# Performance work log

Hardware: AMD Instinct MI355X
Metric: run time of the kernel (lower is better)

Reference implementation:

```python
import jax, jax.numpy as jnp
import numpy as np

B, T, D, N = 256, 512, 512, 64


def setup_inputs() -> dict:
    key = jax.random.key(0)
    ks = jax.random.split(key, 8)
    s = 0.05  # keep gate pre-activations in a sane range
    return {
        "x": jax.random.normal(ks[0], (B, T, D), dtype=jnp.float32),
        "init_h": jax.random.normal(ks[1], (B, D), dtype=jnp.float32) * s,
        "W_ih": jax.random.normal(ks[2], (4 * D, D + N), dtype=jnp.float32) * s,
        "b_ih": jax.random.normal(ks[3], (4 * D,), dtype=jnp.float32) * s,
        "W_hh": jax.random.normal(ks[4], (4 * D, D), dtype=jnp.float32) * s,
        "b_hh": jax.random.normal(ks[5], (4 * D,), dtype=jnp.float32) * s,
        "W_lin": jax.random.normal(ks[6], (N, D), dtype=jnp.float32) * s,
        "b_lin": jax.random.normal(ks[7], (N,), dtype=jnp.float32) * s,
    }


def reference(x, init_h, W_ih, b_ih, W_hh, b_hh, W_lin, b_lin):
    n_class = W_lin.shape[0]
    d = init_h.shape[-1]

    def step(carry, x_t):
        h, c, y = carry
        inp = jnp.concatenate([x_t, y], axis=-1)  # [B, D+N]
        gates = inp @ W_ih.T + b_ih + h @ W_hh.T + b_hh  # [B, 4D]
        i, f, g, o = jnp.split(gates, 4, axis=-1)
        i = jax.nn.sigmoid(i)
        f = jax.nn.sigmoid(f)
        g = jnp.tanh(g)
        o = jax.nn.sigmoid(o)
        c = f * c + i * g
        h = o * jnp.tanh(c)
        y = jax.nn.softmax(h @ W_lin.T + b_lin, axis=-1)  # [B, N]
        return (h, c, y), y

    c0 = jnp.zeros_like(init_h)
    y0 = jnp.zeros((x.shape[0], n_class), dtype=x.dtype)
    xs = jnp.swapaxes(x, 0, 1)  # [T, B, D]
    _, ys = jax.lax.scan(step, (init_h, c0, y0), xs)  # ys: [T, B, N]
    return jnp.swapaxes(ys, 0, 1)  # [B, T, N]
```

## Files before the change

kernel.cpp:

```cpp
#include <hip/hip_runtime.h>
#include <cstdint>
#include <cstddef>


typedef _Float16 f16x8 __attribute__((ext_vector_type(8)));
typedef float f32x4 __attribute__((ext_vector_type(4)));
typedef unsigned long long u64;

#define MFMA16(a, b, c_) __builtin_amdgcn_mfma_f32_16x16x32_f16((a), (b), (c_), 0, 0, 0)
#define AGT __HIP_MEMORY_SCOPE_AGENT
#define RLX __ATOMIC_RELAXED

#define FLAG_INTS (256 * 64 + 64)
#define HS2_U32 131072

static __device__ __forceinline__ unsigned short f2b(_Float16 h) {
  return __builtin_bit_cast(unsigned short, h);
}
static __device__ __forceinline__ _Float16 b2f(unsigned short s) {
  return __builtin_bit_cast(_Float16, s);
}

__device__ __forceinline__ void cvt8(const float4 a, const float4 b, f16x8& hi, f16x8& lo) {
  float v[8] = {a.x, a.y, a.z, a.w, b.x, b.y, b.z, b.w};
#pragma unroll
  for (int j = 0; j < 8; ++j) {
    _Float16 h = (_Float16)v[j];
    hi[j] = h;
    lo[j] = (_Float16)(v[j] - (float)h);
  }
}

template <bool XPRE>
__global__ void prep_kernel(const float* __restrict__ x, const float* __restrict__ init_h,
                            const float* __restrict__ W_ih, const float* __restrict__ b_ih,
                            const float* __restrict__ W_hh, const float* __restrict__ b_hh,
                            const float* __restrict__ W_lin, _Float16* __restrict__ xs,
                            _Float16* __restrict__ wf_hi, _Float16* __restrict__ wf_lo,
                            _Float16* __restrict__ wlf_hi, unsigned int* __restrict__ hs2,
                            float* __restrict__ bias, int* __restrict__ flags) {
  const long NX = XPRE ? 256L * 512 * 16 * 4 : 0;
  const int NWF = 128 * 34 * 64;
  const int NWLF = 4 * 16 * 64;
  const int NH2 = 256 * 128;
  long tid = (long)blockIdx.x * 256 + threadIdx.x;

  if (XPRE && tid < NX) {
    int q = tid & 3, ki = (tid >> 2) & 15, t = (tid >> 6) & 511;
    int row = (int)(tid >> 15);
    const float* s = x + (((size_t)row * 512 + t) * 512 + ki * 32 + 4 * q);
    float4 a = *(const float4*)s, b = *(const float4*)(s + 16);
    f16x8 hi, lo;
    cvt8(a, b, hi, lo);
    _Float16* d = xs + ((((size_t)row * 512 + t) * 16 + ki) * 64 + q * 16);
    *(f16x8*)d = hi;
    *(f16x8*)(d + 8) = lo;
    return;
  }
  long u = tid - NX;
  if (u >= 0 && u < NWF) {
    int l = (int)(u & 63);
    int u2 = (int)(u >> 6);
    int ki = u2 % 34, ct = u2 / 34;
    int cb = ct >> 1, cth = ct & 1;
    int l15 = l & 15;
    int col = (l15 >> 2) * 512 + cb * 8 + cth * 4 + (l15 & 3);
    int k = ki * 32 + 4 * (l >> 4);
    float4 a, b;
    if (k < 512) {
      const float* p = W_ih + (size_t)col * 576;
      a = *(const float4*)(p + k);
      b = *(const float4*)(p + k + 16);
    } else if (k < 1024) {
      const float* p = W_hh + (size_t)col * 512;
      a = *(const float4*)(p + k - 512);
      b = *(const float4*)(p + k - 512 + 16);
    } else {
      const float* p = W_ih + (size_t)col * 576 + 512;
      a = *(const float4*)(p + k - 1024);
      b = *(const float4*)(p + k - 1024 + 16);
    }
    f16x8 hi, lo;
    cvt8(a, b, hi, lo);
    size_t idx = (((size_t)ct * 34 + ki) * 64 + l) * 8;
    *(f16x8*)(wf_hi + idx) = hi;
    *(f16x8*)(wf_lo + idx) = lo;
    return;
  }
  u -= NWF;
  if (u >= 0 && u < NWLF) {
    int l = (int)(u & 63);
    int u2 = (int)(u >> 6);
    int ki = u2 & 15, ct = u2 >> 4;
    int col = ct * 16 + (l & 15);
    int k = ki * 32 + 4 * (l >> 4);
    const float* p = W_lin + (size_t)col * 512;
    float4 a = *(const float4*)(p + k), b = *(const float4*)(p + k + 16);
    f16x8 hi, lo;
    cvt8(a, b, hi, lo);
    _Float16* dh = wlf_hi + ((size_t)(ct * 16 + ki) * 64 + l) * 8;
    *(f16x8*)dh = hi;
    return;
  }
  u -= NWLF;
  if (u >= 0 && u < NH2) {
    int g4 = (int)(u & 127), row = (int)(u >> 7);
    const float* s = init_h + (size_t)row * 512 + g4 * 4;
    float4 a = *(const float4*)s;
    float v[4] = {a.x, a.y, a.z, a.w};
    unsigned int* d = hs2 + (size_t)row * 512 + g4 * 4;
#pragma unroll
    for (int j = 0; j < 4; ++j) {
      _Float16 hh = (_Float16)v[j];
      _Float16 hl = (_Float16)(v[j] - (float)hh);
      d[j] = (unsigned int)f2b(hh) | ((unsigned int)f2b(hl) << 16);
    }
    return;
  }
  u -= NH2;
  if (u >= 0 && u < 2048) {
    bias[u] = b_ih[u] + b_hh[u];
    return;
  }
  u -= 2048;
  if (u >= 0 && u < FLAG_INTS) flags[u] = 0;
}

template <bool XPRE>
__global__ void __launch_bounds__(512, 1) recur_kernel(
    const float* __restrict__ x, const float* __restrict__ b_lin,
    const _Float16* __restrict__ xs, const _Float16* __restrict__ wf_hi,
    const _Float16* __restrict__ wf_lo, const _Float16* __restrict__ wlf_hi,
    unsigned int* __restrict__ hs2, const float* __restrict__ bias, float* __restrict__ out,
    int* __restrict__ flags) {
  const int bid = blockIdx.x;
  const int x8 = bid & 7;
  const int g = x8 >> 1;
  const int cb = (x8 & 1) * 32 + (bid >> 3);
  const int tid = threadIdx.x;
  const int l = tid & 63, w = tid >> 6;
  const int l15 = l & 15, q = l >> 4;
  const int kh = w & 1, rtp = w >> 1;

  __shared__ _Float16 wfl_hi[2 * 34 * 64 * 8];
  __shared__ _Float16 wlin_h[4 * 16 * 64 * 8];
  __shared__ float scratch[4608];
  __shared__ int s_ab;

  {
    const _Float16* srcw = wf_hi + (size_t)(2 * cb) * 17408;
#pragma unroll
    for (int i = 0; i < 9; ++i) {
      int u = tid + i * 512;
      if (u < 4352) *(float4*)(wfl_hi + (size_t)u * 8) = *(const float4*)(srcw + (size_t)u * 8);
    }
#pragma unroll
    for (int i = 0; i < 8; ++i) {
      int u = tid + i * 512;
      *(float4*)(wlin_h + (size_t)u * 8) = *(const float4*)(wlf_hi + (size_t)u * 8);
    }
    if (tid == 0) s_ab = 0;
  }
  __syncthreads();

  const int dd = l15 & 3, rr = l15 >> 2;
  float bg[2][4];
#pragma unroll
  for (int c2 = 0; c2 < 2; ++c2)
#pragma unroll
    for (int gi = 0; gi < 4; ++gi) bg[c2][gi] = bias[gi * 512 + cb * 8 + c2 * 4 + dd];
  const float blv0 = b_lin[l15], blv1 = b_lin[16 + l15];
  const float blv2 = b_lin[32 + l15], blv3 = b_lin[48 + l15];

  const int Rw = g * 64 + rtp * 16;
  const int rowA = Rw + l15;
  const _Float16* xsA = xs + (size_t)rowA * 524288 + q * 16;
  const float* xfA = x + (size_t)rowA * 262144 + 4 * q;
  const unsigned int* hldA = hs2 + (size_t)rowA * 512 + 4 * q;
  const int rowE = Rw + 4 * q + rr;

  const _Float16* wflo_b = wf_lo + (size_t)(2 * cb) * 17408 + (size_t)l * 8;

  int* abortf = flags + 256 * 64;

  auto ARRIVE = [&](int v) {
    __syncthreads();
    if (tid == 0) __hip_atomic_store(flags + (size_t)(g * 64 + cb) * 64, v, RLX, AGT);
  };
  auto WAIT = [&](int v) -> bool {
    if (tid < 64) {
      int a = 0;
      int* f = flags + ((size_t)g * 64 + tid) * 64;
      int it = 0;
      while (__hip_atomic_load(f, RLX, AGT) < v) {
        __builtin_amdgcn_s_sleep(1);
        if (++it > 400000) {
          a = 1;
          break;
        }
        if ((it & 255) == 0 && __hip_atomic_load(abortf, RLX, AGT) != 0) {
          a = 1;
          break;
        }
      }
      a = __any(a) ? 1 : 0;
      if (tid == 0) {
        if (a) __hip_atomic_store(abortf, 1, RLX, AGT);
        s_ab = a;
      }
    }
    __syncthreads();
    return s_ab != 0;
  };

  auto GK3 = [&](const f16x8& ah, const f16x8& al, int KI, f32x4& A0, f32x4& A1) {
    const _Float16* ph0 = wfl_hi + ((size_t)KI * 64 + l) * 8;
    const _Float16* ph1 = ph0 + 17408;
    const _Float16* pl0 = wflo_b + (size_t)KI * 512;
    const _Float16* pl1 = pl0 + 17408;
    f16x8 b0h = *(const f16x8*)ph0, b1h = *(const f16x8*)ph1;
    f16x8 b0l = *(const f16x8*)pl0, b1l = *(const f16x8*)pl1;
    A0 = MFMA16(ah, b0h, A0);
    A1 = MFMA16(ah, b1h, A1);
    A0 = MFMA16(al, b0h, A0);
    A1 = MFMA16(al, b1h, A1);
    A0 = MFMA16(ah, b0l, A0);
    A1 = MFMA16(ah, b1l, A1);
  };
  auto XGEMM = [&](int t, f32x4& A0, f32x4& A1) {
    if (XPRE) {
      const _Float16* xA = xsA + (size_t)t * 1024;
#pragma unroll
      for (int i = 0; i < 8; ++i) {
        int kx = kh * 8 + i;
        f16x8 ah = *(const f16x8*)(xA + kx * 64);
        f16x8 al = *(const f16x8*)(xA + kx * 64 + 8);
        GK3(ah, al, kx, A0, A1);
      }
    } else {
      const float* xp = xfA + (size_t)t * 512;
#pragma unroll 2
      for (int i = 0; i < 8; ++i) {
        int kx = kh * 8 + i;
        float4 av = *(const float4*)(xp + kx * 32);
        float4 bv = *(const float4*)(xp + kx * 32 + 16);
        f16x8 ah, al;
        cvt8(av, bv, ah, al);
        GK3(ah, al, kx, A0, A1);
      }
    }
  };

  const f32x4 Z = {0.f, 0.f, 0.f, 0.f};
  float cst[2] = {0.f, 0.f};
  f32x4 aC0 = Z, aC1 = Z;
  XGEMM(0, aC0, aC1);

  const int ctW = cb >> 4, lW = cb & 15;

#pragma unroll 1
  for (int s = 0; s < 512; ++s) {
    if (s > 0) {
      if (WAIT(s)) return;
    }

    f16x8 hh[8], hl[8];
    const unsigned int* hp0 = hldA + (size_t)(s & 1) * HS2_U32;
#pragma unroll
    for (int i = 0; i < 8; ++i) {
      const unsigned int* hp = hp0 + (kh * 8 + i) * 32;
      u64 u0 = __hip_atomic_load((const u64*)hp, RLX, AGT);
      u64 u1 = __hip_atomic_load((const u64*)(hp + 2), RLX, AGT);
      u64 u2 = __hip_atomic_load((const u64*)(hp + 16), RLX, AGT);
      u64 u3 = __hip_atomic_load((const u64*)(hp + 18), RLX, AGT);
      unsigned int wd[8] = {(unsigned int)u0, (unsigned int)(u0 >> 32),
                            (unsigned int)u1, (unsigned int)(u1 >> 32),
                            (unsigned int)u2, (unsigned int)(u2 >> 32),
                            (unsigned int)u3, (unsigned int)(u3 >> 32)};
#pragma unroll
      for (int j = 0; j < 8; ++j) {
        hh[i][j] = b2f((unsigned short)(wd[j] & 0xffffu));
        hl[i][j] = b2f((unsigned short)(wd[j] >> 16));
      }
    }

    f32x4 y0 = Z, y1 = Z, y2 = Z, y3 = Z;
    if (s > 0) {
#pragma unroll
      for (int i = 0; i < 8; ++i) {
        int ki = kh * 8 + i;
        const _Float16* ph0 = wlin_h + ((size_t)(0 * 16 + ki) * 64 + l) * 8;
        const _Float16* ph1 = wlin_h + ((size_t)(1 * 16 + ki) * 64 + l) * 8;
        const _Float16* ph2 = wlin_h + ((size_t)(2 * 16 + ki) * 64 + l) * 8;
        const _Float16* ph3 = wlin_h + ((size_t)(3 * 16 + ki) * 64 + l) * 8;
        f16x8 b0 = *(const f16x8*)ph0, b1 = *(const f16x8*)ph1;
        f16x8 b2 = *(const f16x8*)ph2, b3 = *(const f16x8*)ph3;
        y0 = MFMA16(hh[i], b0, y0);
        y1 = MFMA16(hh[i], b1, y1);
        y2 = MFMA16(hh[i], b2, y2);
        y3 = MFMA16(hh[i], b3, y3);
        y0 = MFMA16(hl[i], b0, y0);
        y1 = MFMA16(hl[i], b1, y1);
        y2 = MFMA16(hl[i], b2, y2);
        y3 = MFMA16(hl[i], b3, y3);
      }
    }
#pragma unroll
    for (int i = 0; i < 8; ++i) GK3(hh[i], hl[i], 16 + kh * 8 + i, aC0, aC1);

    if (s > 0) {
      if (kh == 1) {
#pragma unroll
        for (int r = 0; r < 4; ++r) {
          scratch[((rtp * 4 + 0) * 4 + r) * 64 + l] = y0[r];
          scratch[((rtp * 4 + 1) * 4 + r) * 64 + l] = y1[r];
          scratch[((rtp * 4 + 2) * 4 + r) * 64 + l] = y2[r];
          scratch[((rtp * 4 + 3) * 4 + r) * 64 + l] = y3[r];
        }
      }
      __syncthreads();
      float la0[4], la1[4], la2[4], la3[4];
      if (kh == 0) {
#pragma unroll
        for (int r = 0; r < 4; ++r) {
          la0[r] = y0[r] + scratch[((rtp * 4 + 0) * 4 + r) * 64 + l] + blv0;
          la1[r] = y1[r] + scratch[((rtp * 4 + 1) * 4 + r) * 64 + l] + blv1;
          la2[r] = y2[r] + scratch[((rtp * 4 + 2) * 4 + r) * 64 + l] + blv2;
          la3[r] = y3[r] + scratch[((rtp * 4 + 3) * 4 + r) * 64 + l] + blv3;
        }
#pragma unroll
        for (int r = 0; r < 4; ++r) {
          float mx = fmaxf(fmaxf(la0[r], la1[r]), fmaxf(la2[r], la3[r]));
          mx = fmaxf(mx, __shfl_xor(mx, 1));
          mx = fmaxf(mx, __shfl_xor(mx, 2));
          mx = fmaxf(mx, __shfl_xor(mx, 4));
          mx = fmaxf(mx, __shfl_xor(mx, 8));
          float e0 = __expf(la0[r] - mx), e1 = __expf(la1[r] - mx);
          float e2 = __expf(la2[r] - mx), e3 = __expf(la3[r] - mx);
          float sm = e0 + e1 + e2 + e3;
          sm += __shfl_xor(sm, 1);
          sm += __shfl_xor(sm, 2);
          sm += __shfl_xor(sm, 4);
          sm += __shfl_xor(sm, 8);
          float inv = 1.f / sm;
          la0[r] = e0 * inv;
          la1[r] = e1 * inv;
          la2[r] = e2 * inv;
          la3[r] = e3 * inv;
        }
        if (l15 == lW) {
#pragma unroll
          for (int r = 0; r < 4; ++r) {
            float vv = (ctW == 0) ? la0[r] : (ctW == 1) ? la1[r] : (ctW == 2) ? la2[r] : la3[r];
            out[((size_t)(g * 64 + rtp * 16 + 4 * q + r) * 512 + (s - 1)) * 64 + cb] = vv;
          }
        }
      }
      __syncthreads();
      if (kh == 0) {
        _Float16* yt = (_Float16*)scratch;
#pragma unroll
        for (int r = 0; r < 4; ++r) {
          int row = rtp * 16 + 4 * q + r;
          float v[4] = {la0[r], la1[r], la2[r], la3[r]};
#pragma unroll
          for (int ct = 0; ct < 4; ++ct) {
            _Float16 vh = (_Float16)v[ct];
            _Float16 vl = (_Float16)(v[ct] - (float)vh);
            yt[row * 136 + ct * 16 + l15] = vh;
            yt[row * 136 + 72 + ct * 16 + l15] = vl;
          }
        }
      }
      __syncthreads();
      {
        const _Float16* yt = (const _Float16*)scratch + (rtp * 16 + l15) * 136 + kh * 32 + 4 * q;
        union {
          u64 d[2];
          f16x8 v;
        } th, tl;
        th.d[0] = *(const u64*)yt;
        th.d[1] = *(const u64*)(yt + 16);
        tl.d[0] = *(const u64*)(yt + 72);
        tl.d[1] = *(const u64*)(yt + 88);
        GK3(th.v, tl.v, 32 + kh, aC0, aC1);
      }
      __syncthreads();
    }

    if (kh == 1) {
#pragma unroll
      for (int r = 0; r < 4; ++r) {
        scratch[((rtp * 2 + 0) * 4 + r) * 64 + l] = aC0[r];
        scratch[((rtp * 2 + 1) * 4 + r) * 64 + l] = aC1[r];
      }
    }
    __syncthreads();
    if (kh == 0) {
#pragma unroll
      for (int r = 0; r < 4; ++r) {
        aC0[r] += scratch[((rtp * 2 + 0) * 4 + r) * 64 + l];
        aC1[r] += scratch[((rtp * 2 + 1) * 4 + r) * 64 + l];
      }
#pragma unroll
      for (int c2 = 0; c2 < 2; ++c2) {
        f32x4 A = c2 ? aC1 : aC0;
        float z[4];
#pragma unroll
        for (int gi = 0; gi < 4; ++gi) {
          int src = (l & 48) | (gi * 4 + dd);
          float v0 = __shfl(A[0], src), v1 = __shfl(A[1], src);
          float v2 = __shfl(A[2], src), v3 = __shfl(A[3], src);
          z[gi] = (rr == 0) ? v0 : (rr == 1) ? v1 : (rr == 2) ? v2 : v3;
        }
        float zi = z[0] + bg[c2][0], zf = z[1] + bg[c2][1];
        float zg = z[2] + bg[c2][2], zo = z[3] + bg[c2][3];
        float iv = 1.f / (1.f + __expf(-zi));
        float fv = 1.f / (1.f + __expf(-zf));
        float eg = __expf(2.f * zg);
        float gv = 1.f - 2.f / (eg + 1.f);
        float ov = 1.f / (1.f + __expf(-zo));
        float cn = fv * cst[c2] + iv * gv;
        cst[c2] = cn;
        float ec = __expf(2.f * cn);
        float th2 = 1.f - 2.f / (ec + 1.f);
        float hv = ov * th2;
        _Float16 hhv = (_Float16)hv;
        _Float16 hlv = (_Float16)(hv - (float)hhv);
        unsigned int pk = (unsigned int)f2b(hhv) | ((unsigned int)f2b(hlv) << 16);
        int dglob = cb * 8 + c2 * 4 + dd;
        __hip_atomic_store(hs2 + (size_t)((s + 1) & 1) * HS2_U32 + rowE * 512 + dglob, pk, RLX,
                           AGT);
      }
    }
    ARRIVE(s + 1);
    if (s < 511) {
      f32x4 aN0 = Z, aN1 = Z;
      XGEMM(s + 1, aN0, aN1);
      aC0 = aN0;
      aC1 = aN1;
    }
  }

  if (WAIT(512)) return;
  {
    f16x8 hh[8], hl[8];
    const unsigned int* hp0 = hldA;
#pragma unroll
    for (int i = 0; i < 8; ++i) {
      const unsigned int* hp = hp0 + (kh * 8 + i) * 32;
      u64 u0 = __hip_atomic_load((const u64*)hp, RLX, AGT);
      u64 u1 = __hip_atomic_load((const u64*)(hp + 2), RLX, AGT);
      u64 u2 = __hip_atomic_load((const u64*)(hp + 16), RLX, AGT);
      u64 u3 = __hip_atomic_load((const u64*)(hp + 18), RLX, AGT);
      unsigned int wd[8] = {(unsigned int)u0, (unsigned int)(u0 >> 32),
                            (unsigned int)u1, (unsigned int)(u1 >> 32),
                            (unsigned int)u2, (unsigned int)(u2 >> 32),
                            (unsigned int)u3, (unsigned int)(u3 >> 32)};
#pragma unroll
      for (int j = 0; j < 8; ++j) {
        hh[i][j] = b2f((unsigned short)(wd[j] & 0xffffu));
        hl[i][j] = b2f((unsigned short)(wd[j] >> 16));
      }
    }
    f32x4 y0 = Z, y1 = Z, y2 = Z, y3 = Z;
#pragma unroll
    for (int i = 0; i < 8; ++i) {
      int ki = kh * 8 + i;
      const _Float16* ph0 = wlin_h + ((size_t)(0 * 16 + ki) * 64 + l) * 8;
      const _Float16* ph1 = wlin_h + ((size_t)(1 * 16 + ki) * 64 + l) * 8;
      const _Float16* ph2 = wlin_h + ((size_t)(2 * 16 + ki) * 64 + l) * 8;
      const _Float16* ph3 = wlin_h + ((size_t)(3 * 16 + ki) * 64 + l) * 8;
      f16x8 b0 = *(const f16x8*)ph0, b1 = *(const f16x8*)ph1;
      f16x8 b2 = *(const f16x8*)ph2, b3 = *(const f16x8*)ph3;
      y0 = MFMA16(hh[i], b0, y0);
      y1 = MFMA16(hh[i], b1, y1);
      y2 = MFMA16(hh[i], b2, y2);
      y3 = MFMA16(hh[i], b3, y3);
      y0 = MFMA16(hl[i], b0, y0);
      y1 = MFMA16(hl[i], b1, y1);
      y2 = MFMA16(hl[i], b2, y2);
      y3 = MFMA16(hl[i], b3, y3);
    }
    if (kh == 1) {
#pragma unroll
      for (int r = 0; r < 4; ++r) {
        scratch[((rtp * 4 + 0) * 4 + r) * 64 + l] = y0[r];
        scratch[((rtp * 4 + 1) * 4 + r) * 64 + l] = y1[r];
        scratch[((rtp * 4 + 2) * 4 + r) * 64 + l] = y2[r];
        scratch[((rtp * 4 + 3) * 4 + r) * 64 + l] = y3[r];
      }
    }
    __syncthreads();
    if (kh == 0) {
      float la0[4], la1[4], la2[4], la3[4];
#pragma unroll
      for (int r = 0; r < 4; ++r) {
        la0[r] = y0[r] + scratch[((rtp * 4 + 0) * 4 + r) * 64 + l] + blv0;
        la1[r] = y1[r] + scratch[((rtp * 4 + 1) * 4 + r) * 64 + l] + blv1;
        la2[r] = y2[r] + scratch[((rtp * 4 + 2) * 4 + r) * 64 + l] + blv2;
        la3[r] = y3[r] + scratch[((rtp * 4 + 3) * 4 + r) * 64 + l] + blv3;
      }
#pragma unroll
      for (int r = 0; r < 4; ++r) {
        float mx = fmaxf(fmaxf(la0[r], la1[r]), fmaxf(la2[r], la3[r]));
        mx = fmaxf(mx, __shfl_xor(mx, 1));
        mx = fmaxf(mx, __shfl_xor(mx, 2));
        mx = fmaxf(mx, __shfl_xor(mx, 4));
        mx = fmaxf(mx, __shfl_xor(mx, 8));
        float e0 = __expf(la0[r] - mx), e1 = __expf(la1[r] - mx);
        float e2 = __expf(la2[r] - mx), e3 = __expf(la3[r] - mx);
        float sm = e0 + e1 + e2 + e3;
        sm += __shfl_xor(sm, 1);
        sm += __shfl_xor(sm, 2);
        sm += __shfl_xor(sm, 4);
        sm += __shfl_xor(sm, 8);
        float inv = 1.f / sm;
        la0[r] = e0 * inv;
        la1[r] = e1 * inv;
        la2[r] = e2 * inv;
        la3[r] = e3 * inv;
      }
      if (l15 == lW) {
#pragma unroll
        for (int r = 0; r < 4; ++r) {
          float vv = (ctW == 0) ? la0[r] : (ctW == 1) ? la1[r] : (ctW == 2) ? la2[r] : la3[r];
          out[((size_t)(g * 64 + rtp * 16 + 4 * q + r) * 512 + 511) * 64 + cb] = vv;
        }
      }
    }
  }
}

extern "C" void kernel_launch(void* const* d_in, const int* in_sizes, int n_in, void* d_out,
                              int out_size, void* d_ws, size_t ws_size, hipStream_t stream) {
  const float* x = (const float*)d_in[0];
  const float* init_h = (const float*)d_in[1];
  const float* W_ih = (const float*)d_in[2];
  const float* b_ih = (const float*)d_in[3];
  const float* W_hh = (const float*)d_in[4];
  const float* b_hh = (const float*)d_in[5];
  const float* W_lin = (const float*)d_in[6];
  const float* b_lin = (const float*)d_in[7];
  float* out = (float*)d_out;
  (void)in_sizes;
  (void)n_in;
  (void)out_size;

  char* ws = (char*)d_ws;
  size_t off = 0;
  auto take = [&](size_t bytes) -> char* {
    char* r = ws + off;
    off = (off + bytes + 255) & ~(size_t)255;
    return r;
  };
  const size_t WFP_E = (size_t)128 * 34 * 64 * 8;
  const size_t WLF_E = (size_t)4 * 16 * 64 * 8;
  const size_t XS_E = (size_t)256 * 512 * 16 * 64;

  _Float16* wf_hi = (_Float16*)take(WFP_E * 2);
  _Float16* wf_lo = (_Float16*)take(WFP_E * 2);
  _Float16* wlf_hi = (_Float16*)take(WLF_E * 2);
  unsigned int* hs2 = (unsigned int*)take((size_t)2 * HS2_U32 * 4);
  float* bias = (float*)take(2048 * 4);
  int* flags = (int*)take((size_t)FLAG_INTS * 4);
  if (ws_size < off) return;
  _Float16* xs = (_Float16*)(ws + off);
  const bool xpre = (ws_size >= off + XS_E * 2);

  if (xpre) {
    const long total = 8388608L + 278528 + 4096 + 32768 + 2048 + FLAG_INTS;
    prep_kernel<true><<<(int)((total + 255) / 256), 256, 0, stream>>>(
        x, init_h, W_ih, b_ih, W_hh, b_hh, W_lin, xs, wf_hi, wf_lo, wlf_hi, hs2, bias, flags);
    recur_kernel<true><<<256, 512, 0, stream>>>(x, b_lin, xs, wf_hi, wf_lo, wlf_hi, hs2, bias,
                                                out, flags);
  } else {
    const long total = 278528L + 4096 + 32768 + 2048 + FLAG_INTS;
    prep_kernel<false><<<(int)((total + 255) / 256), 256, 0, stream>>>(
        x, init_h, W_ih, b_ih, W_hh, b_hh, W_lin, xs, wf_hi, wf_lo, wlf_hi, hs2, bias, flags);
    recur_kernel<false><<<256, 512, 0, stream>>>(x, b_lin, xs, wf_hi, wf_lo, wlf_hi, hs2, bias,
                                                 out, flags);
  }
}
```

Baseline: 9.623 ms.

## Partition LSTM recurrence per XCD with local sync groups and hi/lo LDS weights

Each block reads its XCD id from a hardware register and takes a slot through an atomic counter. Groups of 32 blocks on the same XCD then share batch rows, so the per-step flag barrier and hidden-state exchange stay within one XCD's L2. Recurrent weights (W_hh plus the feedback part of W_ih) are stored interleaved as hi/lo in LDS. The input-projection weights are now read from global memory. The softmax feedback GEMM is done by half the waves, with W_lin read from global. Atomics become volatile accesses and x gets nontemporal loads. The kernel aborts if the XCD mapping does not yield exactly 32 blocks per XCD. It depends on the hardware block placement and on volatile ordering being correct for cross-block visibility.

```diff
diff --git a/kernel.cpp b/kernel.cpp
--- a/kernel.cpp
+++ b/kernel.cpp
@@ -5,14 +5,17 @@
 
 typedef _Float16 f16x8 __attribute__((ext_vector_type(8)));
 typedef float f32x4 __attribute__((ext_vector_type(4)));
+typedef unsigned int u32x4 __attribute__((ext_vector_type(4)));
 typedef unsigned long long u64;
 
 #define MFMA16(a, b, c_) __builtin_amdgcn_mfma_f32_16x16x32_f16((a), (b), (c_), 0, 0, 0)
 #define AGT __HIP_MEMORY_SCOPE_AGENT
 #define RLX __ATOMIC_RELAXED
 
-#define FLAG_INTS (256 * 64 + 64)
 #define HS2_U32 131072
+#define ABORT_OFF 16384
+#define XCDCNT_OFF 16448
+#define FLAG_INTS 16456
 
 static __device__ __forceinline__ unsigned short f2b(_Float16 h) {
   return __builtin_bit_cast(unsigned short, h);
@@ -36,9 +39,10 @@
                             const float* __restrict__ W_ih, const float* __restrict__ b_ih,
                             const float* __restrict__ W_hh, const float* __restrict__ b_hh,
                             const float* __restrict__ W_lin, _Float16* __restrict__ xs,
-                            _Float16* __restrict__ wf_hi, _Float16* __restrict__ wf_lo,
-                            _Float16* __restrict__ wlf_hi, unsigned int* __restrict__ hs2,
-                            float* __restrict__ bias, int* __restrict__ flags) {
+                            _Float16* __restrict__ wx_hi, _Float16* __restrict__ wx_lo,
+                            _Float16* __restrict__ whl, _Float16* __restrict__ wlf_hi,
+                            unsigned int* __restrict__ hs2, float* __restrict__ bias,
+                            int* __restrict__ flags) {
   const long NX = XPRE ? 256L * 512 * 16 * 4 : 0;
   const int NWF = 128 * 34 * 64;
   const int NWLF = 4 * 16 * 64;
@@ -61,10 +65,9 @@
   if (u >= 0 && u < NWF) {
     int l = (int)(u & 63);
     int u2 = (int)(u >> 6);
-    int ki = u2 % 34, ct = u2 / 34;
-    int cb = ct >> 1, cth = ct & 1;
-    int l15 = l & 15;
-    int col = (l15 >> 2) * 512 + cb * 8 + cth * 4 + (l15 & 3);
+    int ki = u2 % 34, sl = u2 / 34;
+    int gate = sl & 3, c = sl >> 2;
+    int col = gate * 512 + c * 16 + (l & 15);
     int k = ki * 32 + 4 * (l >> 4);
     float4 a, b;
     if (k < 512) {
@@ -82,9 +85,15 @@
     }
     f16x8 hi, lo;
     cvt8(a, b, hi, lo);
-    size_t idx = (((size_t)ct * 34 + ki) * 64 + l) * 8;
-    *(f16x8*)(wf_hi + idx) = hi;
-    *(f16x8*)(wf_lo + idx) = lo;
+    if (ki < 16) {
+      size_t idx = (((size_t)sl * 16 + ki) * 64 + l) * 8;
+      *(f16x8*)(wx_hi + idx) = hi;
+      *(f16x8*)(wx_lo + idx) = lo;
+    } else {
+      size_t idx = (((size_t)sl * 18 + (ki - 16)) * 64 + l) * 16;
+      *(f16x8*)(whl + idx) = hi;
+      *(f16x8*)(whl + idx + 8) = lo;
+    }
     return;
   }
   u -= NWF;
@@ -98,8 +107,7 @@
     float4 a = *(const float4*)(p + k), b = *(const float4*)(p + k + 16);
     f16x8 hi, lo;
     cvt8(a, b, hi, lo);
-    _Float16* dh = wlf_hi + ((size_t)(ct * 16 + ki) * 64 + l) * 8;
-    *(f16x8*)dh = hi;
+    *(f16x8*)(wlf_hi + ((size_t)(ct * 16 + ki) * 64 + l) * 8) = hi;
     return;
   }
   u -= NWLF;
@@ -129,72 +137,70 @@
 template <bool XPRE>
 __global__ void __launch_bounds__(512, 1) recur_kernel(
     const float* __restrict__ x, const float* __restrict__ b_lin,
-    const _Float16* __restrict__ xs, const _Float16* __restrict__ wf_hi,
-    const _Float16* __restrict__ wf_lo, const _Float16* __restrict__ wlf_hi,
-    unsigned int* __restrict__ hs2, const float* __restrict__ bias, float* __restrict__ out,
-    int* __restrict__ flags) {
-  const int bid = blockIdx.x;
-  const int x8 = bid & 7;
-  const int g = x8 >> 1;
-  const int cb = (x8 & 1) * 32 + (bid >> 3);
+    const _Float16* __restrict__ xs, const _Float16* __restrict__ wx_hi,
+    const _Float16* __restrict__ wx_lo, const _Float16* __restrict__ whl,
+    const _Float16* __restrict__ wlf_hi, unsigned int* __restrict__ hs2,
+    const float* __restrict__ bias, float* __restrict__ out, int* __restrict__ flags) {
   const int tid = threadIdx.x;
   const int l = tid & 63, w = tid >> 6;
   const int l15 = l & 15, q = l >> 4;
-  const int kh = w & 1, rtp = w >> 1;
-
-  __shared__ _Float16 wfl_hi[2 * 34 * 64 * 8];
-  __shared__ _Float16 wlin_h[4 * 16 * 64 * 8];
-  __shared__ float scratch[4608];
-  __shared__ int s_ab;
+  const int kh = w & 1, rt = (w >> 1) & 1, ch = w >> 2;
+
+  __shared__ _Float16 whl_lds[73728];
+  __shared__ float scratch[2304];
+  __shared__ int s_ab, s_g, s_c;
+
+  if (tid == 0) {
+    s_ab = 0;
+    int xcc = __builtin_amdgcn_s_getreg(63508) & 7;
+    int slot = __hip_atomic_fetch_add(flags + XCDCNT_OFF + xcc, 1, RLX, AGT);
+    s_g = xcc;
+    s_c = slot;
+    if (slot >= 32) {
+      __hip_atomic_store(flags + ABORT_OFF, 1, RLX, AGT);
+      s_ab = 1;
+    }
+  }
+  __syncthreads();
+  if (s_ab) return;
+  const int g = s_g, c = s_c;
+  const int ct0 = ch * 2, ct1 = ch * 2 + 1;
 
   {
-    const _Float16* srcw = wf_hi + (size_t)(2 * cb) * 17408;
-#pragma unroll
-    for (int i = 0; i < 9; ++i) {
-      int u = tid + i * 512;
-      if (u < 4352) *(float4*)(wfl_hi + (size_t)u * 8) = *(const float4*)(srcw + (size_t)u * 8);
-    }
-#pragma unroll
-    for (int i = 0; i < 8; ++i) {
-      int u = tid + i * 512;
-      *(float4*)(wlin_h + (size_t)u * 8) = *(const float4*)(wlf_hi + (size_t)u * 8);
-    }
-    if (tid == 0) s_ab = 0;
+    const _Float16* src = whl + (size_t)c * 73728;
+#pragma unroll
+    for (int i = 0; i < 18; ++i) {
+      int uu = tid + i * 512;
+      *(float4*)(whl_lds + (size_t)uu * 8) = *(const float4*)(src + (size_t)uu * 8);
+    }
   }
   __syncthreads();
 
-  const int dd = l15 & 3, rr = l15 >> 2;
-  float bg[2][4];
-#pragma unroll
-  for (int c2 = 0; c2 < 2; ++c2)
-#pragma unroll
-    for (int gi = 0; gi < 4; ++gi) bg[c2][gi] = bias[gi * 512 + cb * 8 + c2 * 4 + dd];
+  float bg[4];
+#pragma unroll
+  for (int gi = 0; gi < 4; ++gi) bg[gi] = bias[gi * 512 + c * 16 + l15];
   const float blv0 = b_lin[l15], blv1 = b_lin[16 + l15];
   const float blv2 = b_lin[32 + l15], blv3 = b_lin[48 + l15];
 
-  const int Rw = g * 64 + rtp * 16;
-  const int rowA = Rw + l15;
+  const int rowA = g * 32 + rt * 16 + l15;
   const _Float16* xsA = xs + (size_t)rowA * 524288 + q * 16;
   const float* xfA = x + (size_t)rowA * 262144 + 4 * q;
   const unsigned int* hldA = hs2 + (size_t)rowA * 512 + 4 * q;
-  const int rowE = Rw + 4 * q + rr;
-
-  const _Float16* wflo_b = wf_lo + (size_t)(2 * cb) * 17408 + (size_t)l * 8;
-
-  int* abortf = flags + 256 * 64;
+
+  int* abortf = flags + ABORT_OFF;
 
   auto ARRIVE = [&](int v) {
     __syncthreads();
-    if (tid == 0) __hip_atomic_store(flags + (size_t)(g * 64 + cb) * 64, v, RLX, AGT);
+    if (tid == 0) *(volatile int*)(flags + (size_t)(g * 32 + c) * 64) = v;
   };
   auto WAIT = [&](int v) -> bool {
-    if (tid < 64) {
+    if (tid < 32) {
       int a = 0;
-      int* f = flags + ((size_t)g * 64 + tid) * 64;
+      volatile int* f = (volatile int*)(flags + ((size_t)g * 32 + tid) * 64);
       int it = 0;
-      while (__hip_atomic_load(f, RLX, AGT) < v) {
+      while (*f < v) {
         __builtin_amdgcn_s_sleep(1);
-        if (++it > 400000) {
+        if (++it > 300000) {
           a = 1;
           break;
         }
@@ -213,13 +219,23 @@
     return s_ab != 0;
   };
 
-  auto GK3 = [&](const f16x8& ah, const f16x8& al, int KI, f32x4& A0, f32x4& A1) {
-    const _Float16* ph0 = wfl_hi + ((size_t)KI * 64 + l) * 8;
-    const _Float16* ph1 = ph0 + 17408;
-    const _Float16* pl0 = wflo_b + (size_t)KI * 512;
-    const _Float16* pl1 = pl0 + 17408;
-    f16x8 b0h = *(const f16x8*)ph0, b1h = *(const f16x8*)ph1;
-    f16x8 b0l = *(const f16x8*)pl0, b1l = *(const f16x8*)pl1;
+  auto GKH = [&](const f16x8& ah, const f16x8& al, int kidx, f32x4& A0, f32x4& A1) {
+    const _Float16* p0 = whl_lds + (((size_t)ct0 * 18 + kidx) * 64 + l) * 16;
+    const _Float16* p1 = whl_lds + (((size_t)ct1 * 18 + kidx) * 64 + l) * 16;
+    f16x8 b0h = *(const f16x8*)p0, b0l = *(const f16x8*)(p0 + 8);
+    f16x8 b1h = *(const f16x8*)p1, b1l = *(const f16x8*)(p1 + 8);
+    A0 = MFMA16(ah, b0h, A0);
+    A1 = MFMA16(ah, b1h, A1);
+    A0 = MFMA16(al, b0h, A0);
+    A1 = MFMA16(al, b1h, A1);
+    A0 = MFMA16(ah, b0l, A0);
+    A1 = MFMA16(ah, b1l, A1);
+  };
+  auto GKX = [&](const f16x8& ah, const f16x8& al, int ki, f32x4& A0, f32x4& A1) {
+    size_t i0 = (((size_t)(c * 4 + ct0) * 16 + ki) * 64 + l) * 8;
+    size_t i1 = (((size_t)(c * 4 + ct1) * 16 + ki) * 64 + l) * 8;
+    f16x8 b0h = *(const f16x8*)(wx_hi + i0), b0l = *(const f16x8*)(wx_lo + i0);
+    f16x8 b1h = *(const f16x8*)(wx_hi + i1), b1l = *(const f16x8*)(wx_lo + i1);
     A0 = MFMA16(ah, b0h, A0);
     A1 = MFMA16(ah, b1h, A1);
     A0 = MFMA16(al, b0h, A0);
@@ -233,9 +249,13 @@
 #pragma unroll
       for (int i = 0; i < 8; ++i) {
         int kx = kh * 8 + i;
-        f16x8 ah = *(const f16x8*)(xA + kx * 64);
-        f16x8 al = *(const f16x8*)(xA + kx * 64 + 8);
-        GK3(ah, al, kx, A0, A1);
+        union {
+          u32x4 u;
+          f16x8 v;
+        } ua, ub;
+        ua.u = __builtin_nontemporal_load((const u32x4*)(xA + kx * 64));
+        ub.u = __builtin_nontemporal_load((const u32x4*)(xA + kx * 64 + 8));
+        GKX(ua.v, ub.v, kx, A0, A1);
       }
     } else {
       const float* xp = xfA + (size_t)t * 512;
@@ -246,17 +266,15 @@
         float4 bv = *(const float4*)(xp + kx * 32 + 16);
         f16x8 ah, al;
         cvt8(av, bv, ah, al);
-        GK3(ah, al, kx, A0, A1);
+        GKX(ah, al, kx, A0, A1);
       }
     }
   };
 
   const f32x4 Z = {0.f, 0.f, 0.f, 0.f};
-  float cst[2] = {0.f, 0.f};
+  float cst[4] = {0.f, 0.f, 0.f, 0.f};
   f32x4 aC0 = Z, aC1 = Z;
   XGEMM(0, aC0, aC1);
-
-  const int ctW = cb >> 4, lW = cb & 15;
 
 #pragma unroll 1
   for (int s = 0; s < 512; ++s) {
@@ -269,10 +287,10 @@
 #pragma unroll
     for (int i = 0; i < 8; ++i) {
       const unsigned int* hp = hp0 + (kh * 8 + i) * 32;
-      u64 u0 = __hip_atomic_load((const u64*)hp, RLX, AGT);
-      u64 u1 = __hip_atomic_load((const u64*)(hp + 2), RLX, AGT);
-      u64 u2 = __hip_atomic_load((const u64*)(hp + 16), RLX, AGT);
-      u64 u3 = __hip_atomic_load((const u64*)(hp + 18), RLX, AGT);
+      u64 u0 = *(const volatile u64*)hp;
+      u64 u1 = *(const volatile u64*)(hp + 2);
+      u64 u2 = *(const volatile u64*)(hp + 16);
+      u64 u3 = *(const volatile u64*)(hp + 18);
       unsigned int wd[8] = {(unsigned int)u0, (unsigned int)(u0 >> 32),
                             (unsigned int)u1, (unsigned int)(u1 >> 32),
                             (unsigned int)u2, (unsigned int)(u2 >> 32),
@@ -285,16 +303,14 @@
     }
 
     f32x4 y0 = Z, y1 = Z, y2 = Z, y3 = Z;
-    if (s > 0) {
+    if (s > 0 && ch == 0) {
 #pragma unroll
       for (int i = 0; i < 8; ++i) {
         int ki = kh * 8 + i;
-        const _Float16* ph0 = wlin_h + ((size_t)(0 * 16 + ki) * 64 + l) * 8;
-        const _Float16* ph1 = wlin_h + ((size_t)(1 * 16 + ki) * 64 + l) * 8;
-        const _Float16* ph2 = wlin_h + ((size_t)(2 * 16 + ki) * 64 + l) * 8;
-        const _Float16* ph3 = wlin_h + ((size_t)(3 * 16 + ki) * 64 + l) * 8;
-        f16x8 b0 = *(const f16x8*)ph0, b1 = *(const f16x8*)ph1;
-        f16x8 b2 = *(const f16x8*)ph2, b3 = *(const f16x8*)ph3;
+        f16x8 b0 = *(const f16x8*)(wlf_hi + (((size_t)(0 * 16 + ki)) * 64 + l) * 8);
+        f16x8 b1 = *(const f16x8*)(wlf_hi + (((size_t)(1 * 16 + ki)) * 64 + l) * 8);
+        f16x8 b2 = *(const f16x8*)(wlf_hi + (((size_t)(2 * 16 + ki)) * 64 + l) * 8);
+        f16x8 b3 = *(const f16x8*)(wlf_hi + (((size_t)(3 * 16 + ki)) * 64 + l) * 8);
         y0 = MFMA16(hh[i], b0, y0);
         y1 = MFMA16(hh[i], b1, y1);
         y2 = MFMA16(hh[i], b2, y2);
@@ -306,67 +322,66 @@
       }
     }
 #pragma unroll
-    for (int i = 0; i < 8; ++i) GK3(hh[i], hl[i], 16 + kh * 8 + i, aC0, aC1);
+    for (int i = 0; i < 8; ++i) GKH(hh[i], hl[i], kh * 8 + i, aC0, aC1);
 
     if (s > 0) {
-      if (kh == 1) {
+      if (ch == 0 && kh == 1) {
 #pragma unroll
         for (int r = 0; r < 4; ++r) {
-          scratch[((rtp * 4 + 0) * 4 + r) * 64 + l] = y0[r];
-          scratch[((rtp * 4 + 1) * 4 + r) * 64 + l] = y1[r];
-          scratch[((rtp * 4 + 2) * 4 + r) * 64 + l] = y2[r];
-          scratch[((rtp * 4 + 3) * 4 + r) * 64 + l] = y3[r];
+          scratch[((rt * 4 + 0) * 4 + r) * 64 + l] = y0[r];
+          scratch[((rt * 4 + 1) * 4 + r) * 64 + l] = y1[r];
+          scratch[((rt * 4 + 2) * 4 + r) * 64 + l] = y2[r];
+          scratch[((rt * 4 + 3) * 4 + r) * 64 + l] = y3[r];
         }
       }
       __syncthreads();
-      float la0[4], la1[4], la2[4], la3[4];
-      if (kh == 0) {
+      if (ch == 0 && kh == 0) {
+        float la[4][4];
 #pragma unroll
         for (int r = 0; r < 4; ++r) {
-          la0[r] = y0[r] + scratch[((rtp * 4 + 0) * 4 + r) * 64 + l] + blv0;
-          la1[r] = y1[r] + scratch[((rtp * 4 + 1) * 4 + r) * 64 + l] + blv1;
-          la2[r] = y2[r] + scratch[((rtp * 4 + 2) * 4 + r) * 64 + l] + blv2;
-          la3[r] = y3[r] + scratch[((rtp * 4 + 3) * 4 + r) * 64 + l] + blv3;
+          la[0][r] = y0[r] + scratch[((rt * 4 + 0) * 4 + r) * 64 + l] + blv0;
+          la[1][r] = y1[r] + scratch[((rt * 4 + 1) * 4 + r) * 64 + l] + blv1;
+          la[2][r] = y2[r] + scratch[((rt * 4 + 2) * 4 + r) * 64 + l] + blv2;
+          la[3][r] = y3[r] + scratch[((rt * 4 + 3) * 4 + r) * 64 + l] + blv3;
         }
 #pragma unroll
         for (int r = 0; r < 4; ++r) {
-          float mx = fmaxf(fmaxf(la0[r], la1[r]), fmaxf(la2[r], la3[r]));
+          float mx = fmaxf(fmaxf(la[0][r], la[1][r]), fmaxf(la[2][r], la[3][r]));
           mx = fmaxf(mx, __shfl_xor(mx, 1));
           mx = fmaxf(mx, __shfl_xor(mx, 2));
           mx = fmaxf(mx, __shfl_xor(mx, 4));
           mx = fmaxf(mx, __shfl_xor(mx, 8));
-          float e0 = __expf(la0[r] - mx), e1 = __expf(la1[r] - mx);
-          float e2 = __expf(la2[r] - mx), e3 = __expf(la3[r] - mx);
+          float e0 = __expf(la[0][r] - mx), e1 = __expf(la[1][r] - mx);
+          float e2 = __expf(la[2][r] - mx), e3 = __expf(la[3][r] - mx);
           float sm = e0 + e1 + e2 + e3;
           sm += __shfl_xor(sm, 1);
           sm += __shfl_xor(sm, 2);
           sm += __shfl_xor(sm, 4);
           sm += __shfl_xor(sm, 8);
           float inv = 1.f / sm;
-          la0[r] = e0 * inv;
-          la1[r] = e1 * inv;
-          la2[r] = e2 * inv;
-          la3[r] = e3 * inv;
-        }
-        if (l15 == lW) {
-#pragma unroll
-          for (int r = 0; r < 4; ++r) {
-            float vv = (ctW == 0) ? la0[r] : (ctW == 1) ? la1[r] : (ctW == 2) ? la2[r] : la3[r];
-            out[((size_t)(g * 64 + rtp * 16 + 4 * q + r) * 512 + (s - 1)) * 64 + cb] = vv;
+          la[0][r] = e0 * inv;
+          la[1][r] = e1 * inv;
+          la[2][r] = e2 * inv;
+          la[3][r] = e3 * inv;
+        }
+#pragma unroll
+        for (int j2 = 0; j2 < 2; ++j2) {
+          int n = 2 * c + j2;
+          if (l15 == (n & 15)) {
+#pragma unroll
+            for (int r = 0; r < 4; ++r)
+              out[((size_t)(g * 32 + rt * 16 + 4 * q + r) * 512 + (s - 1)) * 64 + n] =
+                  la[n >> 4][r];
           }
         }
-      }
-      __syncthreads();
-      if (kh == 0) {
         _Float16* yt = (_Float16*)scratch;
 #pragma unroll
         for (int r = 0; r < 4; ++r) {
-          int row = rtp * 16 + 4 * q + r;
-          float v[4] = {la0[r], la1[r], la2[r], la3[r]};
+          int row = rt * 16 + 4 * q + r;
 #pragma unroll
           for (int ct = 0; ct < 4; ++ct) {
-            _Float16 vh = (_Float16)v[ct];
-            _Float16 vl = (_Float16)(v[ct] - (float)vh);
+            _Float16 vh = (_Float16)la[ct][r];
+            _Float16 vl = (_Float16)(la[ct][r] - (float)vh);
             yt[row * 136 + ct * 16 + l15] = vh;
             yt[row * 136 + 72 + ct * 16 + l15] = vl;
           }
@@ -374,7 +389,7 @@
       }
       __syncthreads();
       {
-        const _Float16* yt = (const _Float16*)scratch + (rtp * 16 + l15) * 136 + kh * 32 + 4 * q;
+        const _Float16* yt = (const _Float16*)scratch + (rt * 16 + l15) * 136 + kh * 32 + 4 * q;
         union {
           u64 d[2];
           f16x8 v;
@@ -383,7 +398,7 @@
         th.d[1] = *(const u64*)(yt + 16);
         tl.d[0] = *(const u64*)(yt + 72);
         tl.d[1] = *(const u64*)(yt + 88);
-        GK3(th.v, tl.v, 32 + kh, aC0, aC1);
+        GKH(th.v, tl.v, 16 + kh, aC0, aC1);
       }
       __syncthreads();
     }
@@ -391,46 +406,50 @@
     if (kh == 1) {
 #pragma unroll
       for (int r = 0; r < 4; ++r) {
-        scratch[((rtp * 2 + 0) * 4 + r) * 64 + l] = aC0[r];
-        scratch[((rtp * 2 + 1) * 4 + r) * 64 + l] = aC1[r];
+        scratch[((rt * 4 + ct0) * 4 + r) * 64 + l] = aC0[r];
+        scratch[((rt * 4 + ct1) * 4 + r) * 64 + l] = aC1[r];
       }
     }
     __syncthreads();
     if (kh == 0) {
 #pragma unroll
       for (int r = 0; r < 4; ++r) {
-        aC0[r] += scratch[((rtp * 2 + 0) * 4 + r) * 64 + l];
-        aC1[r] += scratch[((rtp * 2 + 1) * 4 + r) * 64 + l];
-      }
-#pragma unroll
-      for (int c2 = 0; c2 < 2; ++c2) {
-        f32x4 A = c2 ? aC1 : aC0;
-        float z[4];
-#pragma unroll
-        for (int gi = 0; gi < 4; ++gi) {
-          int src = (l & 48) | (gi * 4 + dd);
-          float v0 = __shfl(A[0], src), v1 = __shfl(A[1], src);
-          float v2 = __shfl(A[2], src), v3 = __shfl(A[3], src);
-          z[gi] = (rr == 0) ? v0 : (rr == 1) ? v1 : (rr == 2) ? v2 : v3;
-        }
-        float zi = z[0] + bg[c2][0], zf = z[1] + bg[c2][1];
-        float zg = z[2] + bg[c2][2], zo = z[3] + bg[c2][3];
+        aC0[r] += scratch[((rt * 4 + ct0) * 4 + r) * 64 + l];
+        aC1[r] += scratch[((rt * 4 + ct1) * 4 + r) * 64 + l];
+      }
+      if (ch == 1) {
+#pragma unroll
+        for (int r = 0; r < 4; ++r) {
+          scratch[((rt * 4 + 2) * 4 + r) * 64 + l] = aC0[r];
+          scratch[((rt * 4 + 3) * 4 + r) * 64 + l] = aC1[r];
+        }
+      }
+    }
+    __syncthreads();
+    if (kh == 0 && ch == 0) {
+      const unsigned int wbuf = (unsigned int)(((s + 1) & 1) * HS2_U32);
+      const int dglob = c * 16 + l15;
+#pragma unroll
+      for (int r = 0; r < 4; ++r) {
+        float zi = aC0[r] + bg[0];
+        float zf = aC1[r] + bg[1];
+        float zg = scratch[((rt * 4 + 2) * 4 + r) * 64 + l] + bg[2];
+        float zo = scratch[((rt * 4 + 3) * 4 + r) * 64 + l] + bg[3];
         float iv = 1.f / (1.f + __expf(-zi));
         float fv = 1.f / (1.f + __expf(-zf));
         float eg = __expf(2.f * zg);
         float gv = 1.f - 2.f / (eg + 1.f);
         float ov = 1.f / (1.f + __expf(-zo));
-        float cn = fv * cst[c2] + iv * gv;
-        cst[c2] = cn;
+        float cn = fv * cst[r] + iv * gv;
+        cst[r] = cn;
         float ec = __expf(2.f * cn);
         float th2 = 1.f - 2.f / (ec + 1.f);
         float hv = ov * th2;
         _Float16 hhv = (_Float16)hv;
         _Float16 hlv = (_Float16)(hv - (float)hhv);
         unsigned int pk = (unsigned int)f2b(hhv) | ((unsigned int)f2b(hlv) << 16);
-        int dglob = cb * 8 + c2 * 4 + dd;
-        __hip_atomic_store(hs2 + (size_t)((s + 1) & 1) * HS2_U32 + rowE * 512 + dglob, pk, RLX,
-                           AGT);
+        int grow = g * 32 + rt * 16 + 4 * q + r;
+        hs2[wbuf + (size_t)grow * 512 + dglob] = pk;
       }
     }
     ARRIVE(s + 1);
@@ -445,14 +464,13 @@
   if (WAIT(512)) return;
   {
     f16x8 hh[8], hl[8];
-    const unsigned int* hp0 = hldA;
 #pragma unroll
     for (int i = 0; i < 8; ++i) {
-      const unsigned int* hp = hp0 + (kh * 8 + i) * 32;
-      u64 u0 = __hip_atomic_load((const u64*)hp, RLX, AGT);
-      u64 u1 = __hip_atomic_load((const u64*)(hp + 2), RLX, AGT);
-      u64 u2 = __hip_atomic_load((const u64*)(hp + 16), RLX, AGT);
-      u64 u3 = __hip_atomic_load((const u64*)(hp + 18), RLX, AGT);
+      const unsigned int* hp = hldA + (kh * 8 + i) * 32;
+      u64 u0 = *(const volatile u64*)hp;
+      u64 u1 = *(const volatile u64*)(hp + 2);
+      u64 u2 = *(const volatile u64*)(hp + 16);
+      u64 u3 = *(const volatile u64*)(hp + 18);
       unsigned int wd[8] = {(unsigned int)u0, (unsigned int)(u0 >> 32),
                             (unsigned int)u1, (unsigned int)(u1 >> 32),
                             (unsigned int)u2, (unsigned int)(u2 >> 32),
@@ -464,68 +482,70 @@
       }
     }
     f32x4 y0 = Z, y1 = Z, y2 = Z, y3 = Z;
-#pragma unroll
-    for (int i = 0; i < 8; ++i) {
-      int ki = kh * 8 + i;
-      const _Float16* ph0 = wlin_h + ((size_t)(0 * 16 + ki) * 64 + l) * 8;
-      const _Float16* ph1 = wlin_h + ((size_t)(1 * 16 + ki) * 64 + l) * 8;
-      const _Float16* ph2 = wlin_h + ((size_t)(2 * 16 + ki) * 64 + l) * 8;
-      const _Float16* ph3 = wlin_h + ((size_t)(3 * 16 + ki) * 64 + l) * 8;
-      f16x8 b0 = *(const f16x8*)ph0, b1 = *(const f16x8*)ph1;
-      f16x8 b2 = *(const f16x8*)ph2, b3 = *(const f16x8*)ph3;
-      y0 = MFMA16(hh[i], b0, y0);
-      y1 = MFMA16(hh[i], b1, y1);
-      y2 = MFMA16(hh[i], b2, y2);
-      y3 = MFMA16(hh[i], b3, y3);
-      y0 = MFMA16(hl[i], b0, y0);
-      y1 = MFMA16(hl[i], b1, y1);
-      y2 = MFMA16(hl[i], b2, y2);
-      y3 = MFMA16(hl[i], b3, y3);
-    }
-    if (kh == 1) {
+    if (ch == 0) {
+#pragma unroll
+      for (int i = 0; i < 8; ++i) {
+        int ki = kh * 8 + i;
+        f16x8 b0 = *(const f16x8*)(wlf_hi + (((size_t)(0 * 16 + ki)) * 64 + l) * 8);
+        f16x8 b1 = *(const f16x8*)(wlf_hi + (((size_t)(1 * 16 + ki)) * 64 + l) * 8);
+        f16x8 b2 = *(const f16x8*)(wlf_hi + (((size_t)(2 * 16 + ki)) * 64 + l) * 8);
+        f16x8 b3 = *(const f16x8*)(wlf_hi + (((size_t)(3 * 16 + ki)) * 64 + l) * 8);
+        y0 = MFMA16(hh[i], b0, y0);
+        y1 = MFMA16(hh[i], b1, y1);
+        y2 = MFMA16(hh[i], b2, y2);
+        y3 = MFMA16(hh[i], b3, y3);
+        y0 = MFMA16(hl[i], b0, y0);
+        y1 = MFMA16(hl[i], b1, y1);
+        y2 = MFMA16(hl[i], b2, y2);
+        y3 = MFMA16(hl[i], b3, y3);
+      }
+      if (kh == 1) {
+#pragma unroll
+        for (int r = 0; r < 4; ++r) {
+          scratch[((rt * 4 + 0) * 4 + r) * 64 + l] = y0[r];
+          scratch[((rt * 4 + 1) * 4 + r) * 64 + l] = y1[r];
+          scratch[((rt * 4 + 2) * 4 + r) * 64 + l] = y2[r];
+          scratch[((rt * 4 + 3) * 4 + r) * 64 + l] = y3[r];
+        }
+      }
+    }
+    __syncthreads();
+    if (ch == 0 && kh == 0) {
+      float la[4][4];
 #pragma unroll
       for (int r = 0; r < 4; ++r) {
-        scratch[((rtp * 4 + 0) * 4 + r) * 64 + l] = y0[r];
-        scratch[((rtp * 4 + 1) * 4 + r) * 64 + l] = y1[r];
-        scratch[((rtp * 4 + 2) * 4 + r) * 64 + l] = y2[r];
-        scratch[((rtp * 4 + 3) * 4 + r) * 64 + l] = y3[r];
-      }
-    }
-    __syncthreads();
-    if (kh == 0) {
-      float la0[4], la1[4], la2[4], la3[4];
+        la[0][r] = y0[r] + scratch[((rt * 4 + 0) * 4 + r) * 64 + l] + blv0;
+        la[1][r] = y1[r] + scratch[((rt * 4 + 1) * 4 + r) * 64 + l] + blv1;
+        la[2][r] = y2[r] + scratch[((rt * 4 + 2) * 4 + r) * 64 + l] + blv2;
+        la[3][r] = y3[r] + scratch[((rt * 4 + 3) * 4 + r) * 64 + l] + blv3;
+      }
 #pragma unroll
       for (int r = 0; r < 4; ++r) {
-        la0[r] = y0[r] + scratch[((rtp * 4 + 0) * 4 + r) * 64 + l] + blv0;
-        la1[r] = y1[r] + scratch[((rtp * 4 + 1) * 4 + r) * 64 + l] + blv1;
-        la2[r] = y2[r] + scratch[((rtp * 4 + 2) * 4 + r) * 64 + l] + blv2;
-        la3[r] = y3[r] + scratch[((rtp * 4 + 3) * 4 + r) * 64 + l] + blv3;
-      }
-#pragma unroll
-      for (int r = 0; r < 4; ++r) {
-        float mx = fmaxf(fmaxf(la0[r], la1[r]), fmaxf(la2[r], la3[r]));
+        float mx = fmaxf(fmaxf(la[0][r], la[1][r]), fmaxf(la[2][r], la[3][r]));
         mx = fmaxf(mx, __shfl_xor(mx, 1));
         mx = fmaxf(mx, __shfl_xor(mx, 2));
         mx = fmaxf(mx, __shfl_xor(mx, 4));
         mx = fmaxf(mx, __shfl_xor(mx, 8));
-        float e0 = __expf(la0[r] - mx), e1 = __expf(la1[r] - mx);
-        float e2 = __expf(la2[r] - mx), e3 = __expf(la3[r] - mx);
+        float e0 = __expf(la[0][r] - mx), e1 = __expf(la[1][r] - mx);
+        float e2 = __expf(la[2][r] - mx), e3 = __expf(la[3][r] - mx);
         float sm = e0 + e1 + e2 + e3;
         sm += __shfl_xor(sm, 1);
         sm += __shfl_xor(sm, 2);
         sm += __shfl_xor(sm, 4);
         sm += __shfl_xor(sm, 8);
         float inv = 1.f / sm;
-        la0[r] = e0 * inv;
-        la1[r] = e1 * inv;
-        la2[r] = e2 * inv;
-        la3[r] = e3 * inv;
-      }
-      if (l15 == lW) {
-#pragma unroll
-        for (int r = 0; r < 4; ++r) {
-          float vv = (ctW == 0) ? la0[r] : (ctW == 1) ? la1[r] : (ctW == 2) ? la2[r] : la3[r];
-          out[((size_t)(g * 64 + rtp * 16 + 4 * q + r) * 512 + 511) * 64 + cb] = vv;
+        la[0][r] = e0 * inv;
+        la[1][r] = e1 * inv;
+        la[2][r] = e2 * inv;
+        la[3][r] = e3 * inv;
+      }
+#pragma unroll
+      for (int j2 = 0; j2 < 2; ++j2) {
+        int n = 2 * c + j2;
+        if (l15 == (n & 15)) {
+#pragma unroll
+          for (int r = 0; r < 4; ++r)
+            out[((size_t)(g * 32 + rt * 16 + 4 * q + r) * 512 + 511) * 64 + n] = la[n >> 4][r];
         }
       }
     }
@@ -554,12 +574,14 @@
     off = (off + bytes + 255) & ~(size_t)255;
     return r;
   };
-  const size_t WFP_E = (size_t)128 * 34 * 64 * 8;
+  const size_t WX_E = (size_t)128 * 16 * 64 * 8;
+  const size_t WHL_E = (size_t)128 * 18 * 64 * 16;
   const size_t WLF_E = (size_t)4 * 16 * 64 * 8;
   const size_t XS_E = (size_t)256 * 512 * 16 * 64;
 
-  _Float16* wf_hi = (_Float16*)take(WFP_E * 2);
-  _Float16* wf_lo = (_Float16*)take(WFP_E * 2);
+  _Float16* wx_hi = (_Float16*)take(WX_E * 2);
+  _Float16* wx_lo = (_Float16*)take(WX_E * 2);
+  _Float16* whl = (_Float16*)take(WHL_E * 2);
   _Float16* wlf_hi = (_Float16*)take(WLF_E * 2);
   unsigned int* hs2 = (unsigned int*)take((size_t)2 * HS2_U32 * 4);
   float* bias = (float*)take(2048 * 4);
@@ -571,14 +593,16 @@
   if (xpre) {
     const long total = 8388608L + 278528 + 4096 + 32768 + 2048 + FLAG_INTS;
     prep_kernel<true><<<(int)((total + 255) / 256), 256, 0, stream>>>(
-        x, init_h, W_ih, b_ih, W_hh, b_hh, W_lin, xs, wf_hi, wf_lo, wlf_hi, hs2, bias, flags);
-    recur_kernel<true><<<256, 512, 0, stream>>>(x, b_lin, xs, wf_hi, wf_lo, wlf_hi, hs2, bias,
-                                                out, flags);
+        x, init_h, W_ih, b_ih, W_hh, b_hh, W_lin, xs, wx_hi, wx_lo, whl, wlf_hi, hs2, bias,
+        flags);
+    recur_kernel<true><<<256, 512, 0, stream>>>(x, b_lin, xs, wx_hi, wx_lo, whl, wlf_hi, hs2,
+                                                bias, out, flags);
   } else {
     const long total = 278528L + 4096 + 32768 + 2048 + FLAG_INTS;
     prep_kernel<false><<<(int)((total + 255) / 256), 256, 0, stream>>>(
-        x, init_h, W_ih, b_ih, W_hh, b_hh, W_lin, xs, wf_hi, wf_lo, wlf_hi, hs2, bias, flags);
-    recur_kernel<false><<<256, 512, 0, stream>>>(x, b_lin, xs, wf_hi, wf_lo, wlf_hi, hs2, bias,
-                                                 out, flags);
+        x, init_h, W_ih, b_ih, W_hh, b_hh, W_lin, xs, wx_hi, wx_lo, whl, wlf_hi, hs2, bias,
+        flags);
+    recur_kernel<false><<<256, 512, 0, stream>>>(x, b_lin, xs, wx_hi, wx_lo, whl, wlf_hi, hs2,
+                                                 bias, out, flags);
   }
 }
```

New measurement: 14.38 ms. +49.4%, slower.
